# Kernel tuning notes

Measured on AMD Instinct MI355X. Metric: run time of the kernel, lower is better.

Reference implementation:

```python
import jax, jax.numpy as jnp
import numpy as np

B, S, HID = 1, 4096, 2048
NH, NKV, HD = 16, 4, 128
BLK, LOCAL, GNB, STRIDE = 64, 4, 2, 4
ROT = 64  # head_dim * rope_partial_rotary_factor(0.5), already even
SCALE = HD ** -0.5
NEG = -1e9


def _block_select(nb):
    """Static local+global key-block selection per query block (mirrors _select_key_blocks)."""
    sels = []
    for bi in range(nb):
        local = list(range(max(0, bi - LOCAL + 1), bi + 1))
        gc = list(range(0, bi + 1, STRIDE))
        if len(gc) > GNB:
            gc = gc[-GNB:]
        if 0 not in gc:
            gc = [0] + gc
        idx = sorted(set(local + gc))
        sels.append([i for i in idx if 0 <= i < nb and i <= bi])
    m = max(len(s) for s in sels)
    idx = np.zeros((nb, m), np.int32)
    valid = np.zeros((nb, m), bool)
    for i, s in enumerate(sels):
        idx[i, :len(s)] = s
        valid[i, :len(s)] = True
    return jnp.asarray(idx), jnp.asarray(valid)


def _rot_half(x):
    h = x.shape[-1] // 2
    return jnp.concatenate([-x[..., h:], x[..., :h]], axis=-1)


def setup_inputs() -> dict:
    key = jax.random.key(0)
    ks = jax.random.split(key, 8)
    w = lambda k, shp: (jax.random.normal(k, shp, jnp.float32) * 0.02)
    return {
        "hidden": jax.random.normal(ks[0], (B, S, HID), jnp.float32),
        "cos": jax.random.uniform(ks[1], (B, S, ROT), jnp.float32, -1.0, 1.0),
        "sin": jax.random.uniform(ks[2], (B, S, ROT), jnp.float32, -1.0, 1.0),
        "Wq": w(ks[3], (HID, NH * HD)),
        "Wk": w(ks[4], (HID, NKV * HD)),
        "Wv": w(ks[5], (HID, NKV * HD)),
        "Wo": w(ks[6], (NH * HD, HID)),
        "attn_mask": jnp.ones((B, S), jnp.float32),
    }


def reference(hidden, cos, sin, Wq, Wk, Wv, Wo, attn_mask):
    b_, s_, _ = hidden.shape
    q = (hidden @ Wq).reshape(b_, s_, NH, HD).transpose(0, 2, 1, 3)   # [B,H,S,d]
    k = (hidden @ Wk).reshape(b_, s_, NKV, HD).transpose(0, 2, 1, 3)  # [B,Hkv,S,d]
    v = (hidden @ Wv).reshape(b_, s_, NKV, HD).transpose(0, 2, 1, 3)

    # partial RoPE on first ROT channels
    c = cos[:, None, :, :]
    sn = sin[:, None, :, :]
    q1, q2 = q[..., :ROT], q[..., ROT:]
    k1, k2 = k[..., :ROT], k[..., ROT:]
    q = jnp.concatenate([q1 * c + _rot_half(q1) * sn, q2], axis=-1)
    k = jnp.concatenate([k1 * c + _rot_half(k1) * sn, k2], axis=-1)

    # repeat_kv (GQA expand: each kv head repeated contiguously)
    rep = NH // NKV
    k = jnp.repeat(k, rep, axis=1)
    v = jnp.repeat(v, rep, axis=1)

    nb = s_ // BLK  # S chosen divisible by BLK (pad_len == 0)
    qb = q.reshape(b_, NH, nb, BLK, HD)
    kb = k.reshape(b_, NH, nb, BLK, HD)
    vb = v.reshape(b_, NH, nb, BLK, HD)

    idx, valid = _block_select(nb)  # [nb, M]
    m = idx.shape[1]
    ksel = kb[:, :, idx]  # [B,H,nb,M,BLK,d]
    vsel = vb[:, :, idx]

    scores = jnp.einsum('bhnqd,bhnmkd->bhnqmk',
                        qb.astype(jnp.float32), ksel.astype(jnp.float32)) * SCALE
    # key-validity (padding) mask, additive as in original
    key_valid = attn_mask.reshape(b_, nb, BLK)
    kvm = key_valid[:, idx]  # [B,nb,M,BLK]
    scores = scores + (1.0 - kvm[:, None, :, None, :, :]) * NEG
    # invalid (padded) selected slots
    scores = jnp.where(valid[None, None, :, None, :, None], scores, NEG)
    # intra-block causal mask on the diagonal block
    intra = jnp.triu(jnp.ones((BLK, BLK), bool), 1)                    # [q,k]
    same = idx == jnp.arange(nb)[:, None]                              # [nb,M]
    diag = same[:, None, :, None] & intra[None, :, None, :]            # [nb,q,M,k]
    scores = jnp.where(diag[None, None], NEG, scores)

    probs = jax.nn.softmax(scores.reshape(b_, NH, nb, BLK, m * BLK), axis=-1)
    vflat = vsel.reshape(b_, NH, nb, m * BLK, HD)
    out = jnp.einsum('bhnqe,bhned->bhnqd', probs.astype(v.dtype), vflat)
    out = out.reshape(b_, NH, s_, HD).transpose(0, 2, 1, 3).reshape(b_, s_, NH * HD)
    return out @ Wo
```

## Files before the change

### kernel.cpp

```cpp
#include <hip/hip_runtime.h>
#include <hip/hip_bf16.h>


typedef short short8 __attribute__((ext_vector_type(8)));
typedef float f32x4  __attribute__((ext_vector_type(4)));

#define NEGV   (-1.0e9f)
#define SCALE  (0.08838834764831845f)

__device__ __forceinline__ void gload16(const void* g, void* l) {
  __builtin_amdgcn_global_load_lds(
      (const __attribute__((address_space(1))) unsigned int*)g,
      (__attribute__((address_space(3))) unsigned int*)l, 16, 0, 0);
}

__device__ __forceinline__ float bf2f(short s) {
  union { unsigned u; float f; } c;
  c.u = ((unsigned)(unsigned short)s) << 16;
  return c.f;
}

__device__ __forceinline__ short f2bf_s(float f) {
  __hip_bfloat16 b = __float2bfloat16(f);
  short s;
  __builtin_memcpy(&s, &b, 2);
  return s;
}

__global__ void prep_all(const float* __restrict__ H, const float* __restrict__ Wq,
                         const float* __restrict__ Wk, const float* __restrict__ Wv,
                         const float* __restrict__ Wo, __hip_bfloat16* __restrict__ X,
                         __hip_bfloat16* __restrict__ Wt, __hip_bfloat16* __restrict__ Wot) {
  __shared__ short tile[64][73];
  const int b = blockIdx.x;
  const int tid = threadIdx.x;
  if (b < 4096) {
    size_t t = (size_t)b * 256 + tid;
    const float* hp = H + t * 8;
    float4 v0 = *(const float4*)hp;
    float4 v1 = *(const float4*)(hp + 4);
    short8 o;
    o[0] = f2bf_s(v0.x); o[1] = f2bf_s(v0.y); o[2] = f2bf_s(v0.z); o[3] = f2bf_s(v0.w);
    o[4] = f2bf_s(v1.x); o[5] = f2bf_s(v1.y); o[6] = f2bf_s(v1.z); o[7] = f2bf_s(v1.w);
    *(short8*)&X[t * 8] = o;
    return;
  }
  const float* src; __hip_bfloat16* dst; int C; int idx;
  int q = b - 4096;
  if (q < 1024)      { src = Wq; dst = Wt;                       C = 2048; idx = q; }
  else if (q < 1280) { src = Wk; dst = Wt + (size_t)2048 * 2048; C = 512;  idx = q - 1024; }
  else if (q < 1536) { src = Wv; dst = Wt + (size_t)2560 * 2048; C = 512;  idx = q - 1280; }
  else               { src = Wo; dst = Wot;                      C = 2048; idx = q - 1536; }
  const int r0 = (idx & 31) * 64, c0 = (idx >> 5) * 64;
  const int c4 = (tid & 15) * 4, rb = tid >> 4;
#pragma unroll
  for (int j = 0; j < 4; ++j) {
    int r = rb + j * 16;
    float4 v = *(const float4*)(src + (size_t)(r0 + r) * C + c0 + c4);
    tile[r][c4 + 0] = f2bf_s(v.x);
    tile[r][c4 + 1] = f2bf_s(v.y);
    tile[r][c4 + 2] = f2bf_s(v.z);
    tile[r][c4 + 3] = f2bf_s(v.w);
  }
  __syncthreads();
  const int cs = (tid & 7) * 8;
#pragma unroll
  for (int it = 0; it < 2; ++it) {
    int cc = (tid >> 3) + it * 32;
    short8 o;
#pragma unroll
    for (int i = 0; i < 8; ++i) o[i] = tile[cs + i][cc];
    *(short8*)&dst[(size_t)(c0 + cc) * 2048 + r0 + cs] = o;
  }
}

__global__ void postproc(const float* __restrict__ cosb, const float* __restrict__ sinb,
                         __hip_bfloat16* __restrict__ Kb,
                         const __hip_bfloat16* __restrict__ Vb, __hip_bfloat16* __restrict__ Vt) {
  __shared__ __hip_bfloat16 tile[64][73];
  int blk = blockIdx.x;
  if (blk < 256) {
    int tk = blk * 256 + threadIdx.x;
    int s = tk >> 4;
    int rem = tk & 15;
    __hip_bfloat16* p = Kb + (size_t)s * 512 + (rem >> 2) * 128 + (rem & 3) * 8;
    const int g8 = (tk & 3) * 8;
    const float* cp = cosb + (size_t)s * 64 + g8;
    const float* sp = sinb + (size_t)s * 64 + g8;
    short8 a = *(const short8*)p;
    short8 b = *(const short8*)(p + 32);
    float ca[8], sa[8], cb[8], sb[8];
    *(float4*)&ca[0] = *(const float4*)cp;        *(float4*)&ca[4] = *(const float4*)(cp + 4);
    *(float4*)&cb[0] = *(const float4*)(cp + 32); *(float4*)&cb[4] = *(const float4*)(cp + 36);
    *(float4*)&sa[0] = *(const float4*)sp;        *(float4*)&sa[4] = *(const float4*)(sp + 4);
    *(float4*)&sb[0] = *(const float4*)(sp + 32); *(float4*)&sb[4] = *(const float4*)(sp + 36);
    short8 oa, ob;
#pragma unroll
    for (int i = 0; i < 8; ++i) {
      float av = bf2f(a[i]), bv = bf2f(b[i]);
      oa[i] = f2bf_s(av * ca[i] - bv * sa[i]);
      ob[i] = f2bf_s(bv * cb[i] + av * sb[i]);
    }
    *(short8*)p = oa;
    *(short8*)(p + 32) = ob;
    return;
  }
  int idx = blk - 256;
  int s0 = (idx & 63) * 64, c0 = (idx >> 6) * 64;
  int c = threadIdx.x & 63, rq = threadIdx.x >> 6;
#pragma unroll
  for (int i = 0; i < 16; ++i) {
    int r = i * 4 + rq;
    tile[r][c] = Vb[(size_t)(s0 + r) * 512 + c0 + c];
  }
  __syncthreads();
#pragma unroll
  for (int i = 0; i < 16; ++i) {
    int cc = i * 4 + rq;
    Vt[(size_t)(c0 + cc) * 4096 + s0 + c] = tile[c][cc];
  }
}

__global__ __launch_bounds__(512, 4) void gemm_qkv2p(
    const __hip_bfloat16* __restrict__ A, const __hip_bfloat16* __restrict__ Bt,
    __hip_bfloat16* __restrict__ Qb, __hip_bfloat16* __restrict__ Kb,
    __hip_bfloat16* __restrict__ Vb) {
  const int K = 2048;
  const int tid = threadIdx.x;
  const int wave = tid >> 6, lane = tid & 63;
  const int l15 = lane & 15, lg = lane >> 4;
  const int bm = blockIdx.x, bn = blockIdx.y;
  const int wm = wave >> 2, wn = wave & 3;

  __shared__ __hip_bfloat16 lds[40960];

  f32x4 acc[4][3] = {};
  const int srow = lane >> 3;
  const int sslot = lane & 7;
  const int scol = (sslot ^ srow) * 8;
  const size_t abase = (size_t)bm * 128 * K;
  const size_t bbase = (size_t)bn * 192 * K;
  const int r3 = l15 & 7;

#define STAGE_A(KO, LBASE)                                                       \
  {                                                                              \
    _Pragma("unroll")                                                            \
    for (int l = 0; l < 2; ++l) {                                                \
      int chunk = l * 8 + wave;                                                  \
      int row = chunk * 8 + srow;                                                \
      gload16(A + abase + (size_t)row * K + (KO) + scol,                         \
              &lds[(LBASE) + chunk * 512]);                                      \
    }                                                                            \
  }
#define STAGE_B(KO, LBASE)                                                       \
  {                                                                              \
    _Pragma("unroll")                                                            \
    for (int l = 0; l < 3; ++l) {                                                \
      int chunk = l * 8 + wave;                                                  \
      int row = chunk * 8 + srow;                                                \
      gload16(Bt + bbase + (size_t)row * K + (KO) + scol,                        \
              &lds[(LBASE) + chunk * 512]);                                      \
    }                                                                            \
  }

  short8 bfr[3][2];
  short8 af[2][2][2];

#define READ_AF(P, H, BA)                                                        \
  {                                                                              \
    _Pragma("unroll")                                                            \
    for (int m2 = 0; m2 < 2; ++m2)                                               \
      _Pragma("unroll")                                                          \
      for (int ks = 0; ks < 2; ++ks) {                                           \
        int row = wm * 64 + ((H) * 2 + m2) * 16 + l15;                           \
        int slot = (ks * 4 + lg) ^ r3;                                           \
        af[P][m2][ks] = *(const short8*)&lds[(BA) + row * 64 + slot * 8];        \
      }                                                                          \
  }

#define READ_BF(BB)                                                              \
  {                                                                              \
    _Pragma("unroll")                                                            \
    for (int ni = 0; ni < 3; ++ni)                                               \
      _Pragma("unroll")                                                          \
      for (int ks = 0; ks < 2; ++ks) {                                           \
        int row = wn * 48 + ni * 16 + l15;                                       \
        int slot = (ks * 4 + lg) ^ r3;                                           \
        bfr[ni][ks] = *(const short8*)&lds[(BB) + row * 64 + slot * 8];          \
      }                                                                          \
  }

#define MFMA_1Q(H, P)                                                            \
  {                                                                              \
    __builtin_amdgcn_s_setprio(1);                                               \
    _Pragma("unroll")                                                            \
    for (int ks = 0; ks < 2; ++ks)                                               \
      _Pragma("unroll")                                                          \
      for (int m2 = 0; m2 < 2; ++m2)                                             \
        _Pragma("unroll")                                                        \
        for (int ni = 0; ni < 3; ++ni)                                           \
          acc[(H) * 2 + m2][ni] = __builtin_amdgcn_mfma_f32_16x16x32_bf16(       \
              af[P][m2][ks], bfr[ni][ks], acc[(H) * 2 + m2][ni], 0, 0, 0);       \
    __builtin_amdgcn_s_setprio(0);                                               \
  }

#define LGKM0()                                                                  \
  asm volatile("s_waitcnt lgkmcnt(0)" ::: "memory");                             \
  __builtin_amdgcn_sched_barrier(0);

  STAGE_B(0, 8192);
  STAGE_A(0, 0);
  STAGE_B(64, 20480 + 8192);
  asm volatile("s_waitcnt vmcnt(3)" ::: "memory");
  __builtin_amdgcn_sched_barrier(0);
  __builtin_amdgcn_s_barrier();
  {
    READ_BF(8192);
    READ_AF(0, 0, 0);
  }
  LGKM0();

  for (int t = 0; t < 32; ++t) {
    const int buf = (t & 1) * 20480;
    const int nbuf = buf ^ 20480;
    if (t + 1 < 32) STAGE_A((t + 1) * 64, nbuf);
    __builtin_amdgcn_s_barrier();
    MFMA_1Q(0, 0);
    READ_AF(1, 1, buf);
    LGKM0();
    if (t + 2 < 32) STAGE_B((t + 2) * 64, buf + 8192);
    if (t < 30) asm volatile("s_waitcnt vmcnt(3)" ::: "memory");
    else        asm volatile("s_waitcnt vmcnt(0)" ::: "memory");
    __builtin_amdgcn_sched_barrier(0);
    __builtin_amdgcn_s_barrier();
    MFMA_1Q(1, 1);
    if (t + 1 < 32) {
      READ_BF(nbuf + 8192);
      READ_AF(0, 0, nbuf);
    }
    LGKM0();
  }
#undef STAGE_A
#undef STAGE_B

#pragma unroll
  for (int m4 = 0; m4 < 4; ++m4)
#pragma unroll
    for (int ni = 0; ni < 3; ++ni) {
      int colg = bn * 192 + wn * 48 + ni * 16;
      __hip_bfloat16* dst; int ldc, col;
      if (colg < 2048)      { dst = Qb; ldc = 2048; col = colg + l15; }
      else if (colg < 2560) { dst = Kb; ldc = 512;  col = colg - 2048 + l15; }
      else                  { dst = Vb; ldc = 512;  col = colg - 2560 + l15; }
      int row = bm * 128 + wm * 64 + m4 * 16 + lg * 4;
#pragma unroll
      for (int r = 0; r < 4; ++r)
        dst[(size_t)(row + r) * ldc + col] = __float2bfloat16(acc[m4][ni][r]);
    }
#undef READ_AF
#undef READ_BF
#undef MFMA_1Q
#undef LGKM0
}

__global__ __launch_bounds__(512, 4) void gemm_out2p(
    const __hip_bfloat16* __restrict__ A, const __hip_bfloat16* __restrict__ Bt,
    float* __restrict__ C) {
  const int K = 2048, N = 2048;
  const int tid = threadIdx.x;
  const int wave = tid >> 6, lane = tid & 63;
  const int l15 = lane & 15, lg = lane >> 4;
  const int bm = blockIdx.x, bn = blockIdx.y;
  const int wm = wave >> 2, wn = wave & 3;

  __shared__ __hip_bfloat16 lds[32768];

  f32x4 acc[4][2] = {};
  const int srow = lane >> 3;
  const int sslot = lane & 7;
  const int scol = (sslot ^ srow) * 8;
  const size_t abase = (size_t)bm * 128 * K;
  const size_t bbase = (size_t)bn * 128 * K;
  const int r3 = l15 & 7;

#define STAGE_A(KO, LBASE)                                                       \
  {                                                                              \
    _Pragma("unroll")                                                            \
    for (int l = 0; l < 2; ++l) {                                                \
      int chunk = l * 8 + wave;                                                  \
      int row = chunk * 8 + srow;                                                \
      gload16(A + abase + (size_t)row * K + (KO) + scol,                         \
              &lds[(LBASE) + chunk * 512]);                                      \
    }                                                                            \
  }
#define STAGE_B(KO, LBASE)                                                       \
  {                                                                              \
    _Pragma("unroll")                                                            \
    for (int l = 0; l < 2; ++l) {                                                \
      int chunk = l * 8 + wave;                                                  \
      int row = chunk * 8 + srow;                                                \
      gload16(Bt + bbase + (size_t)row * K + (KO) + scol,                        \
              &lds[(LBASE) + chunk * 512]);                                      \
    }                                                                            \
  }

  short8 bfr[2][2];
  short8 af[2][2][2];

#define READ_AF(P, H, BA)                                                        \
  {                                                                              \
    _Pragma("unroll")                                                            \
    for (int m2 = 0; m2 < 2; ++m2)                                               \
      _Pragma("unroll")                                                          \
      for (int ks = 0; ks < 2; ++ks) {                                           \
        int row = wm * 64 + ((H) * 2 + m2) * 16 + l15;                           \
        int slot = (ks * 4 + lg) ^ r3;                                           \
        af[P][m2][ks] = *(const short8*)&lds[(BA) + row * 64 + slot * 8];        \
      }                                                                          \
  }

#define READ_BF(BB)                                                              \
  {                                                                              \
    _Pragma("unroll")                                                            \
    for (int ni = 0; ni < 2; ++ni)                                               \
      _Pragma("unroll")                                                          \
      for (int ks = 0; ks < 2; ++ks) {                                           \
        int row = wn * 32 + ni * 16 + l15;                                       \
        int slot = (ks * 4 + lg) ^ r3;                                           \
        bfr[ni][ks] = *(const short8*)&lds[(BB) + row * 64 + slot * 8];          \
      }                                                                          \
  }

#define MFMA_1Q(H, P)                                                            \
  {                                                                              \
    __builtin_amdgcn_s_setprio(1);                                               \
    _Pragma("unroll")                                                            \
    for (int ks = 0; ks < 2; ++ks)                                               \
      _Pragma("unroll")                                                          \
      for (int m2 = 0; m2 < 2; ++m2)                                             \
        _Pragma("unroll")                                                        \
        for (int ni = 0; ni < 2; ++ni)                                           \
          acc[(H) * 2 + m2][ni] = __builtin_amdgcn_mfma_f32_16x16x32_bf16(       \
              af[P][m2][ks], bfr[ni][ks], acc[(H) * 2 + m2][ni], 0, 0, 0);       \
    __builtin_amdgcn_s_setprio(0);                                               \
  }

#define LGKM0()                                                                  \
  asm volatile("s_waitcnt lgkmcnt(0)" ::: "memory");                             \
  __builtin_amdgcn_sched_barrier(0);

  STAGE_B(0, 8192);
  STAGE_A(0, 0);
  STAGE_B(64, 16384 + 8192);
  asm volatile("s_waitcnt vmcnt(2)" ::: "memory");
  __builtin_amdgcn_sched_barrier(0);
  __builtin_amdgcn_s_barrier();
  {
    READ_BF(8192);
    READ_AF(0, 0, 0);
  }
  LGKM0();

  for (int t = 0; t < 32; ++t) {
    const int buf = (t & 1) * 16384;
    const int nbuf = buf ^ 16384;
    if (t + 1 < 32) STAGE_A((t + 1) * 64, nbuf);
    __builtin_amdgcn_s_barrier();
    MFMA_1Q(0, 0);
    READ_AF(1, 1, buf);
    LGKM0();
    if (t + 2 < 32) STAGE_B((t + 2) * 64, buf + 8192);
    if (t < 30) asm volatile("s_waitcnt vmcnt(2)" ::: "memory");
    else        asm volatile("s_waitcnt vmcnt(0)" ::: "memory");
    __builtin_amdgcn_sched_barrier(0);
    __builtin_amdgcn_s_barrier();
    MFMA_1Q(1, 1);
    if (t + 1 < 32) {
      READ_BF(nbuf + 8192);
      READ_AF(0, 0, nbuf);
    }
    LGKM0();
  }
#undef STAGE_A
#undef STAGE_B
#undef READ_AF
#undef READ_BF
#undef MFMA_1Q
#undef LGKM0

#pragma unroll
  for (int m4 = 0; m4 < 4; ++m4)
#pragma unroll
    for (int ni = 0; ni < 2; ++ni) {
      int row = bm * 128 + wm * 64 + m4 * 16 + lg * 4;
      int col = bn * 128 + wn * 32 + ni * 16 + l15;
#pragma unroll
      for (int r = 0; r < 4; ++r)
        C[(size_t)(row + r) * N + col] = acc[m4][ni][r];
    }
}

__global__ __launch_bounds__(512, 2) void attn_kernel(
    const __hip_bfloat16* __restrict__ Qb,
    const __hip_bfloat16* __restrict__ Kb,
    const __hip_bfloat16* __restrict__ Vt,
    const float* __restrict__ cosb, const float* __restrict__ sinb,
    const float* __restrict__ amask,
    __hip_bfloat16* __restrict__ AO)
{
  const int bid = blockIdx.x;
  const int kvh = bid & 3;
  const int bi  = bid >> 2;
  const int tid = threadIdx.x;
  const int wave = tid >> 6, lane = tid & 63;
  const int l15 = lane & 15, lg = lane >> 4;
  const int h  = kvh * 4 + (wave >> 1);
  const int rh = wave & 1;
  const int q0 = bi * 64 + rh * 32;

  int sel[6]; int nsel = 0;
  {
    int gtop = bi >> 2;
    for (int j = 0; j <= bi; ++j) {
      bool pick = (j == 0) || (j >= bi - 3) || (((j & 3) == 0) && ((j >> 2) >= gtop - 1));
      if (pick && nsel < 6) sel[nsel++] = j;
    }
  }

  __shared__ __hip_bfloat16 kv[2][16384];
  __shared__ __hip_bfloat16 Pl[8][2304];

  short8 qf[2][4];
#pragma unroll
  for (int mi = 0; mi < 2; ++mi) {
    const int s_ = q0 + mi * 16 + l15;
    const __hip_bfloat16* qrow = Qb + (size_t)s_ * 2048 + h * 128;
#pragma unroll
    for (int ks = 0; ks < 4; ++ks)
      qf[mi][ks] = *(const short8*)(qrow + ks * 32 + lg * 8);
    const float* cp = cosb + (size_t)s_ * 64 + lg * 8;
    const float* sp = sinb + (size_t)s_ * 64 + lg * 8;
    float ca[8], sa[8], cb[8], sb[8];
    *(float4*)&ca[0] = *(const float4*)cp;        *(float4*)&ca[4] = *(const float4*)(cp + 4);
    *(float4*)&cb[0] = *(const float4*)(cp + 32); *(float4*)&cb[4] = *(const float4*)(cp + 36);
    *(float4*)&sa[0] = *(const float4*)sp;        *(float4*)&sa[4] = *(const float4*)(sp + 4);
    *(float4*)&sb[0] = *(const float4*)(sp + 32); *(float4*)&sb[4] = *(const float4*)(sp + 36);
    short8 a = qf[mi][0], b = qf[mi][1], oa, ob;
#pragma unroll
    for (int i = 0; i < 8; ++i) {
      float av = bf2f(a[i]), bv = bf2f(b[i]);
      oa[i] = f2bf_s(av * ca[i] - bv * sa[i]);
      ob[i] = f2bf_s(bv * cb[i] + av * sb[i]);
    }
    qf[mi][0] = oa;
    qf[mi][1] = ob;
  }

  float m[2][4], l[2][4];
  f32x4 oacc[2][8] = {};
#pragma unroll
  for (int mi = 0; mi < 2; ++mi)
#pragma unroll
    for (int r = 0; r < 4; ++r) { m[mi][r] = -3.0e38f; l[mi][r] = 0.f; }

#define STAGE_KV(KB, BUF)                                                          \
  {                                                                                \
    _Pragma("unroll")                                                              \
    for (int i = 0; i < 2; ++i) {                                                  \
      int chunk = (i * 8 + wave) * 64 + lane;                                      \
      int row = chunk >> 4, slot = chunk & 15;                                     \
      gload16(Kb + (size_t)((KB) * 64 + row) * 512 + kvh * 128 +                   \
                  ((slot ^ (row & 15)) * 8),                                       \
              &kv[BUF][(i * 8 + wave) * 512]);                                     \
    }                                                                              \
    _Pragma("unroll")                                                              \
    for (int i = 0; i < 2; ++i) {                                                  \
      int chunk = (i * 8 + wave) * 64 + lane;                                      \
      int row = chunk >> 3, slot = chunk & 7;                                      \
      gload16(Vt + (size_t)(kvh * 128 + row) * 4096 + (KB) * 64 +                  \
                  ((slot ^ (row & 7)) * 8),                                        \
              &kv[BUF][8192 + (i * 8 + wave) * 512]);                              \
    }                                                                              \
  }

  STAGE_KV(sel[0], 0);

#pragma unroll
  for (int j = 0; j < 6; ++j) {
    if (j < nsel) {
      const int kb = sel[j];
      if (j + 1 < nsel) {
        STAGE_KV(sel[j + 1], (j + 1) & 1);
        asm volatile("s_waitcnt vmcnt(4)" ::: "memory");
      } else {
        asm volatile("s_waitcnt vmcnt(0)" ::: "memory");
      }
      __builtin_amdgcn_sched_barrier(0);
      __builtin_amdgcn_s_barrier();
      const __hip_bfloat16* kbuf = kv[j & 1];

      f32x4 sc[2][4] = {};
#pragma unroll
      for (int nf = 0; nf < 4; ++nf)
#pragma unroll
        for (int ks = 0; ks < 4; ++ks) {
          short8 b = *(const short8*)&kbuf[(nf * 16 + l15) * 128 +
                                           (((ks * 4 + lg) ^ l15) * 8)];
          sc[0][nf] = __builtin_amdgcn_mfma_f32_16x16x32_bf16(qf[0][ks], b, sc[0][nf], 0, 0, 0);
          sc[1][nf] = __builtin_amdgcn_mfma_f32_16x16x32_bf16(qf[1][ks], b, sc[1][nf], 0, 0, 0);
        }

      float am[4];
#pragma unroll
      for (int nf = 0; nf < 4; ++nf)
        am[nf] = (1.0f - amask[kb * 64 + nf * 16 + l15]) * NEGV;
#pragma unroll
      for (int mi = 0; mi < 2; ++mi)
#pragma unroll
        for (int nf = 0; nf < 4; ++nf) {
          int keyl = nf * 16 + l15;
#pragma unroll
          for (int r = 0; r < 4; ++r) {
            float s = sc[mi][nf][r] * SCALE + am[nf];
            if (kb == bi) {
              int qrow = rh * 32 + mi * 16 + lg * 4 + r;
              if (keyl > qrow) s = NEGV;
            }
            sc[mi][nf][r] = s;
          }
        }

      float pm[2][4];
#pragma unroll
      for (int mi = 0; mi < 2; ++mi)
#pragma unroll
        for (int r = 0; r < 4; ++r) {
          float v = fmaxf(fmaxf(sc[mi][0][r], sc[mi][1][r]),
                          fmaxf(sc[mi][2][r], sc[mi][3][r]));
          v = fmaxf(v, __shfl_xor(v, 1)); v = fmaxf(v, __shfl_xor(v, 2));
          v = fmaxf(v, __shfl_xor(v, 4)); v = fmaxf(v, __shfl_xor(v, 8));
          pm[mi][r] = v;
        }

      bool need = false;
#pragma unroll
      for (int mi = 0; mi < 2; ++mi)
#pragma unroll
        for (int r = 0; r < 4; ++r) need |= (pm[mi][r] - m[mi][r] > 8.0f);
      if (__any(need)) {
#pragma unroll
        for (int mi = 0; mi < 2; ++mi)
#pragma unroll
          for (int r = 0; r < 4; ++r) {
            float mn = fmaxf(m[mi][r], pm[mi][r]);
            float scl = __expf(m[mi][r] - mn);
            l[mi][r] *= scl;
#pragma unroll
            for (int df = 0; df < 8; ++df) oacc[mi][df][r] *= scl;
            m[mi][r] = mn;
          }
      }

#pragma unroll
      for (int mi = 0; mi < 2; ++mi)
#pragma unroll
        for (int r = 0; r < 4; ++r) {
          float rs = 0.f;
#pragma unroll
          for (int nf = 0; nf < 4; ++nf) {
            float p = __expf(sc[mi][nf][r] - m[mi][r]);
            rs += p;
            Pl[wave][(mi * 16 + lg * 4 + r) * 72 + nf * 16 + l15] = __float2bfloat16(p);
          }
          rs += __shfl_xor(rs, 1); rs += __shfl_xor(rs, 2);
          rs += __shfl_xor(rs, 4); rs += __shfl_xor(rs, 8);
          l[mi][r] += rs;
        }

      short8 af2[2][2];
#pragma unroll
      for (int mi = 0; mi < 2; ++mi)
#pragma unroll
        for (int ks = 0; ks < 2; ++ks)
          af2[mi][ks] = *(const short8*)&Pl[wave][(mi * 16 + l15) * 72 + ks * 32 + lg * 8];
#pragma unroll
      for (int df = 0; df < 8; ++df)
#pragma unroll
        for (int ks = 0; ks < 2; ++ks) {
          short8 vb = *(const short8*)&kbuf[8192 + (df * 16 + l15) * 64 +
                                            (((ks * 4 + lg) ^ (l15 & 7)) * 8)];
          oacc[0][df] = __builtin_amdgcn_mfma_f32_16x16x32_bf16(af2[0][ks], vb, oacc[0][df], 0, 0, 0);
          oacc[1][df] = __builtin_amdgcn_mfma_f32_16x16x32_bf16(af2[1][ks], vb, oacc[1][df], 0, 0, 0);
        }
      __builtin_amdgcn_s_barrier();
    }
  }
#undef STAGE_KV

#pragma unroll
  for (int mi = 0; mi < 2; ++mi) {
    float inv[4];
#pragma unroll
    for (int r = 0; r < 4; ++r) inv[r] = 1.0f / l[mi][r];
#pragma unroll
    for (int df = 0; df < 8; ++df)
#pragma unroll
      for (int r = 0; r < 4; ++r) {
        int qrow = q0 + mi * 16 + lg * 4 + r;
        AO[(size_t)qrow * 2048 + h * 128 + df * 16 + l15] =
            __float2bfloat16(oacc[mi][df][r] * inv[r]);
      }
  }
}

extern "C" void kernel_launch(void* const* d_in, const int* in_sizes, int n_in,
                              void* d_out, int out_size, void* d_ws, size_t ws_size,
                              hipStream_t stream) {
  const float* hidden = (const float*)d_in[0];
  const float* cosb   = (const float*)d_in[1];
  const float* sinb   = (const float*)d_in[2];
  const float* Wq     = (const float*)d_in[3];
  const float* Wk     = (const float*)d_in[4];
  const float* Wv     = (const float*)d_in[5];
  const float* Wo     = (const float*)d_in[6];
  const float* amask  = (const float*)d_in[7];

  char* ws = (char*)d_ws;
  __hip_bfloat16* Xb   = (__hip_bfloat16*)(ws);
  __hip_bfloat16* Wt   = (__hip_bfloat16*)(ws + 16777216);
  __hip_bfloat16* Wot  = (__hip_bfloat16*)(ws + 29360128);
  __hip_bfloat16* Qb   = (__hip_bfloat16*)(ws + 37748736);
  __hip_bfloat16* Kb   = (__hip_bfloat16*)(ws + 54525952);
  __hip_bfloat16* Vb   = (__hip_bfloat16*)(ws + 58720256);
  __hip_bfloat16* Vt   = (__hip_bfloat16*)(ws + 62914560);
  __hip_bfloat16* AO   = Xb;

  prep_all<<<6656, 256, 0, stream>>>(hidden, Wq, Wk, Wv, Wo, Xb, Wt, Wot);

  gemm_qkv2p<<<dim3(32, 16), 512, 0, stream>>>(Xb, Wt, Qb, Kb, Vb);

  postproc<<<768, 256, 0, stream>>>(cosb, sinb, Kb, Vb, Vt);

  attn_kernel<<<256, 512, 0, stream>>>(Qb, Kb, Vt, cosb, sinb, amask, AO);

  gemm_out2p<<<dim3(32, 16), 512, 0, stream>>>(AO, Wot, (float*)d_out);
}
```

Baseline: 150.8 us.

## Enlarge output GEMM tile to 256x128 so A and B fragments are reused more

The output projection GEMM now gives each block a 256x128 tile instead of 128x128, and each wave accumulates a 128x32 sub-tile. Every B fragment read from LDS now feeds twice as many MFMAs, and the grid drops to 256 blocks, one per CU. The cost is more LDS per block (96KB), more accumulator registers, lower occupancy and fewer blocks to hide latency. Staging A now issues more global-to-LDS loads per step under the same vmcnt thresholds.

```diff
diff --git a/kernel.cpp b/kernel.cpp
--- a/kernel.cpp
+++ b/kernel.cpp
@@ -263,7 +263,7 @@
 #undef LGKM0
 }
 
-__global__ __launch_bounds__(512, 4) void gemm_out2p(
+__global__ __launch_bounds__(512, 2) void gemm_out2p(
     const __hip_bfloat16* __restrict__ A, const __hip_bfloat16* __restrict__ Bt,
     float* __restrict__ C) {
   const int K = 2048, N = 2048;
@@ -273,23 +273,23 @@
   const int bm = blockIdx.x, bn = blockIdx.y;
   const int wm = wave >> 2, wn = wave & 3;
 
-  __shared__ __hip_bfloat16 lds[32768];
-
-  f32x4 acc[4][2] = {};
+  __shared__ __hip_bfloat16 lds[49152];
+
+  f32x4 acc[8][2] = {};
   const int srow = lane >> 3;
   const int sslot = lane & 7;
   const int scol = (sslot ^ srow) * 8;
-  const size_t abase = (size_t)bm * 128 * K;
+  const size_t abase = (size_t)bm * 256 * K;
   const size_t bbase = (size_t)bn * 128 * K;
   const int r3 = l15 & 7;
 
-#define STAGE_A(KO, LBASE)                                                       \
+#define STAGE_A(HALF, KO, LBASE)                                                 \
   {                                                                              \
     _Pragma("unroll")                                                            \
     for (int l = 0; l < 2; ++l) {                                                \
       int chunk = l * 8 + wave;                                                  \
       int row = chunk * 8 + srow;                                                \
-      gload16(A + abase + (size_t)row * K + (KO) + scol,                         \
+      gload16(A + abase + (size_t)((HALF) * 128 + row) * K + (KO) + scol,        \
               &lds[(LBASE) + chunk * 512]);                                      \
     }                                                                            \
   }
@@ -307,13 +307,13 @@
   short8 bfr[2][2];
   short8 af[2][2][2];
 
-#define READ_AF(P, H, BA)                                                        \
+#define READ_AF(P, Q, BA)                                                        \
   {                                                                              \
     _Pragma("unroll")                                                            \
     for (int m2 = 0; m2 < 2; ++m2)                                               \
       _Pragma("unroll")                                                          \
       for (int ks = 0; ks < 2; ++ks) {                                           \
-        int row = wm * 64 + ((H) * 2 + m2) * 16 + l15;                           \
+        int row = ((Q) * 2 + m2) * 16 + l15;                                     \
         int slot = (ks * 4 + lg) ^ r3;                                           \
         af[P][m2][ks] = *(const short8*)&lds[(BA) + row * 64 + slot * 8];        \
       }                                                                          \
@@ -331,7 +331,7 @@
       }                                                                          \
   }
 
-#define MFMA_1Q(H, P)                                                            \
+#define MFMA_2Q(QA, QB)                                                          \
   {                                                                              \
     __builtin_amdgcn_s_setprio(1);                                               \
     _Pragma("unroll")                                                            \
@@ -339,9 +339,12 @@
       _Pragma("unroll")                                                          \
       for (int m2 = 0; m2 < 2; ++m2)                                             \
         _Pragma("unroll")                                                        \
-        for (int ni = 0; ni < 2; ++ni)                                           \
-          acc[(H) * 2 + m2][ni] = __builtin_amdgcn_mfma_f32_16x16x32_bf16(       \
-              af[P][m2][ks], bfr[ni][ks], acc[(H) * 2 + m2][ni], 0, 0, 0);       \
+        for (int ni = 0; ni < 2; ++ni) {                                         \
+          acc[(QA) * 2 + m2][ni] = __builtin_amdgcn_mfma_f32_16x16x32_bf16(      \
+              af[0][m2][ks], bfr[ni][ks], acc[(QA) * 2 + m2][ni], 0, 0, 0);      \
+          acc[(QB) * 2 + m2][ni] = __builtin_amdgcn_mfma_f32_16x16x32_bf16(      \
+              af[1][m2][ks], bfr[ni][ks], acc[(QB) * 2 + m2][ni], 0, 0, 0);      \
+        }                                                                        \
     __builtin_amdgcn_s_setprio(0);                                               \
   }
 
@@ -349,35 +352,40 @@
   asm volatile("s_waitcnt lgkmcnt(0)" ::: "memory");                             \
   __builtin_amdgcn_sched_barrier(0);
 
-  STAGE_B(0, 8192);
-  STAGE_A(0, 0);
-  STAGE_B(64, 16384 + 8192);
+  STAGE_B(0, 16384);
+  STAGE_A(0, 0, 0);
+  STAGE_A(1, 0, 8192);
+  STAGE_B(64, 24576 + 16384);
   asm volatile("s_waitcnt vmcnt(2)" ::: "memory");
   __builtin_amdgcn_sched_barrier(0);
   __builtin_amdgcn_s_barrier();
   {
-    READ_BF(8192);
-    READ_AF(0, 0, 0);
+    READ_BF(16384);
+    READ_AF(0, 0, wm * 8192);
+    READ_AF(1, 1, wm * 8192);
   }
   LGKM0();
 
   for (int t = 0; t < 32; ++t) {
-    const int buf = (t & 1) * 16384;
-    const int nbuf = buf ^ 16384;
-    if (t + 1 < 32) STAGE_A((t + 1) * 64, nbuf);
+    const int buf = (t & 1) * 24576;
+    const int nbuf = buf ^ 24576;
+    const int bA = buf + wm * 8192;
+    if (t + 1 < 32) { STAGE_A(0, (t + 1) * 64, nbuf); STAGE_A(1, (t + 1) * 64, nbuf + 8192); }
     __builtin_amdgcn_s_barrier();
-    MFMA_1Q(0, 0);
-    READ_AF(1, 1, buf);
+    MFMA_2Q(0, 1);
+    READ_AF(0, 2, bA);
+    READ_AF(1, 3, bA);
     LGKM0();
-    if (t + 2 < 32) STAGE_B((t + 2) * 64, buf + 8192);
+    if (t + 2 < 32) STAGE_B((t + 2) * 64, buf + 16384);
     if (t < 30) asm volatile("s_waitcnt vmcnt(2)" ::: "memory");
     else        asm volatile("s_waitcnt vmcnt(0)" ::: "memory");
     __builtin_amdgcn_sched_barrier(0);
     __builtin_amdgcn_s_barrier();
-    MFMA_1Q(1, 1);
+    MFMA_2Q(2, 3);
     if (t + 1 < 32) {
-      READ_BF(nbuf + 8192);
-      READ_AF(0, 0, nbuf);
+      READ_BF(nbuf + 16384);
+      READ_AF(0, 0, nbuf + wm * 8192);
+      READ_AF(1, 1, nbuf + wm * 8192);
     }
     LGKM0();
   }
@@ -385,18 +393,18 @@
 #undef STAGE_B
 #undef READ_AF
 #undef READ_BF
-#undef MFMA_1Q
+#undef MFMA_2Q
 #undef LGKM0
 
 #pragma unroll
-  for (int m4 = 0; m4 < 4; ++m4)
+  for (int m8 = 0; m8 < 8; ++m8)
 #pragma unroll
     for (int ni = 0; ni < 2; ++ni) {
-      int row = bm * 128 + wm * 64 + m4 * 16 + lg * 4;
+      int row = bm * 256 + wm * 128 + m8 * 16 + lg * 4;
       int col = bn * 128 + wn * 32 + ni * 16 + l15;
 #pragma unroll
       for (int r = 0; r < 4; ++r)
-        C[(size_t)(row + r) * N + col] = acc[m4][ni][r];
+        C[(size_t)(row + r) * N + col] = acc[m8][ni][r];
     }
 }
 
@@ -643,5 +651,5 @@
 
   attn_kernel<<<256, 512, 0, stream>>>(Qb, Kb, Vt, cosb, sinb, amask, AO);
 
-  gemm_out2p<<<dim3(32, 16), 512, 0, stream>>>(AO, Wot, (float*)d_out);
-}
+  gemm_out2p<<<dim3(16, 16), 512, 0, stream>>>(AO, Wot, (float*)d_out);
+}
```

After: 150.4 us. Within noise of the previous version (-0.2%).
